# Optimization experiments

Measured on AMD Instinct MI355X. Metric: run time of the kernel, lower is better.

The kernel has to match this reference:

```python
import jax, jax.numpy as jnp
import numpy as np


def setup_inputs() -> dict:
    key = jax.random.key(0)
    k1, k2, k3 = jax.random.split(key, 3)
    B, c_in, T, N = 16, 64, 64, 512
    K, c_out = 3, 64
    x = jax.random.normal(k1, (B, c_in, T, N), dtype=jnp.float32)
    # scaled Laplacian-like matrix; scale to keep Chebyshev recurrence stable
    La = jax.random.normal(k2, (B, N, N), dtype=jnp.float32) / jnp.sqrt(jnp.float32(N))
    # Conv2d(K*c_in, c_out, 1x1, bias=False) weight, squeezed to [c_out, K*c_in]
    W = jax.random.normal(k3, (c_out, K * c_in), dtype=jnp.float32) * 0.05
    return {"x": x, "La": La, "W": W}


def reference(x, La, W):
    # x: [B, c_in, T, N], La: [B, N, N], W: [c_out, K*c_in]
    B, c_in, T, N = x.shape
    K = W.shape[1] // c_in
    xp = jnp.transpose(x, (0, 1, 3, 2))  # [B, c_in, N, T] -> 'bcnl'
    # Chebyshev polynomial recurrence: T0 = I, T1 = La, Tk = 2*La@T_{k-1} - T_{k-2}
    I = jnp.broadcast_to(jnp.eye(N, dtype=x.dtype), (B, N, N))
    Ls = [I, La]
    L0, L1 = I, La
    for _ in range(2, K):
        L2 = 2.0 * jnp.matmul(La, L1) - L0
        L0, L1 = L1, L2
        Ls.append(L2)
    Lap = jnp.stack(Ls, axis=1)            # [B, K, N, N]
    Lap = jnp.swapaxes(Lap, -1, -2)        # transpose(-1,-2) as in torch
    # graph conv: contract over source node n
    y = jnp.einsum('bcnl,bknq->bckql', xp, Lap)  # [B, c_in, K, N, T]
    y = y.reshape(B, c_in * K, N, T)       # channel index = c*K + k
    # 1x1 conv, no bias: [c_out, c_in*K] x [B, c_in*K, N, T]
    out = jnp.einsum('oi,binl->bonl', W, y)  # [B, c_out, N, T]
    out = jnp.transpose(out, (0, 1, 3, 2))   # [B, c_out, T, N]
    return out
```

## Files before the change

kernel.cpp:

```cpp
#include <hip/hip_runtime.h>
#include <hip/hip_bf16.h>


#define B_   16
#define CIN  64
#define T_   64
#define N_   512
#define M_   4096
#define KDIM 512
#define COUT 64

typedef __bf16 bf16x8 __attribute__((ext_vector_type(8)));
typedef float  floatx4 __attribute__((ext_vector_type(4)));

__device__ __forceinline__ float bf2f(unsigned short u) {
    unsigned int v = ((unsigned int)u) << 16;
    return __builtin_bit_cast(float, v);
}
__device__ __forceinline__ unsigned short f2bf(float f) {
    unsigned int u = __builtin_bit_cast(unsigned int, f);
    unsigned int lsb = (u >> 16) & 1u;
    u += 0x7fffu + lsb;
    return (unsigned short)(u >> 16);
}

#define GLOAD_LDS16(gp, lp)                                                  \
    __builtin_amdgcn_global_load_lds(                                        \
        (const __attribute__((address_space(1))) void*)(gp),                 \
        (__attribute__((address_space(3))) void*)(lp), 16, 0, 0)

__global__ __launch_bounds__(256) void cvt_f32_bf16(
    const float* __restrict__ src, unsigned short* __restrict__ dst, int n)
{
    int i = (blockIdx.x * 256 + threadIdx.x) * 8;
    if (i + 8 <= n) {
        float4 a = *(const float4*)(src + i);
        float4 b = *(const float4*)(src + i + 4);
        union { unsigned short s[8]; uint4 u; } o;
        o.s[0] = f2bf(a.x); o.s[1] = f2bf(a.y); o.s[2] = f2bf(a.z); o.s[3] = f2bf(a.w);
        o.s[4] = f2bf(b.x); o.s[5] = f2bf(b.y); o.s[6] = f2bf(b.z); o.s[7] = f2bf(b.w);
        *(uint4*)(dst + i) = o.u;
    }
}

__global__ __launch_bounds__(256) void cvt_la_dual(
    const float* __restrict__ La,
    unsigned short* __restrict__ Lab,
    unsigned short* __restrict__ LaT)
{
    __shared__ unsigned short t64[64][68];
    int b  = blockIdx.z;
    int r0 = blockIdx.y * 64;
    int c0 = blockIdx.x * 64;
    int t   = threadIdx.x;
    int row = t >> 2;
    int cg  = (t & 3) * 16;

    const float* src = La + (size_t)b * N_ * N_ + (size_t)(r0 + row) * N_ + c0 + cg;
    unsigned short s[16];
#pragma unroll
    for (int u = 0; u < 4; u++) {
        float4 f = *(const float4*)(src + u * 4);
        s[u * 4 + 0] = f2bf(f.x); s[u * 4 + 1] = f2bf(f.y);
        s[u * 4 + 2] = f2bf(f.z); s[u * 4 + 3] = f2bf(f.w);
    }
    union { unsigned short h[8]; uint4 u; } p0, p1;
#pragma unroll
    for (int u = 0; u < 8; u++) { p0.h[u] = s[u]; p1.h[u] = s[8 + u]; }
    unsigned short* d0 = Lab + (size_t)b * N_ * N_ + (size_t)(r0 + row) * N_ + c0 + cg;
    *(uint4*)d0 = p0.u;
    *(uint4*)(d0 + 8) = p1.u;
#pragma unroll
    for (int u = 0; u < 16; u++) t64[row][cg + u] = s[u];
    __syncthreads();
    int col = t >> 2;
    int rg  = (t & 3) * 16;
    union { unsigned short h[8]; uint4 u; } q0, q1;
#pragma unroll
    for (int u = 0; u < 8; u++) { q0.h[u] = t64[rg + u][col]; q1.h[u] = t64[rg + 8 + u][col]; }
    unsigned short* d1 = LaT + (size_t)b * N_ * N_ + (size_t)(c0 + col) * N_ + r0 + rg;
    *(uint4*)d1 = q0.u;
    *(uint4*)(d1 + 8) = q1.u;
}

__global__ __launch_bounds__(256) void pack_w(
    const float* __restrict__ W, unsigned short* __restrict__ Wb)
{
    int idx = threadIdx.x + blockIdx.x * 256;
    if (idx < 64 * 192) {
        int o = idx / 192, j = idx % 192;
        int c = j & 63, k = j >> 6;
        Wb[idx] = f2bf(W[o * 192 + c * 3 + k]);
    }
}

#define BM 128
#define BN 128
#define BK 32
#define KIT  (KDIM / BK)
#define SBUF (BM * BK)

__global__ __launch_bounds__(256) void gemm_la2(
    const unsigned short* __restrict__ A,
    const unsigned short* __restrict__ Bm,
    unsigned short* __restrict__ C)
{
    int h     = blockIdx.x;
    int g     = h & 7;
    int idx   = h >> 3;
    int batch = g * 2 + (idx >> 4);
    int local = idx & 15;
    int n0    = (local & 3) * BN;
    int m0    = (local >> 2) * BM;

    A  += (size_t)batch * N_ * KDIM;
    Bm += (size_t)batch * N_ * KDIM;
    C  += (size_t)batch * N_ * N_;

    __shared__ __align__(16) unsigned short As[3 * SBUF];
    __shared__ __align__(16) unsigned short Bs[3 * SBUF];

    int tid  = threadIdx.x;
    int lane = tid & 63;
    int wave = tid >> 6;
    int wm   = (wave >> 1) * 64;
    int wn   = (wave & 1) * 64;
    int l15  = lane & 15;
    int quad = lane >> 4;

    int r16 = lane >> 2;
    int sch = lane & 3;
    int gch = sch ^ ((r16 >> 1) & 3);

    const unsigned short* gA0 = A  + (size_t)(m0 + wave * 16 + r16) * KDIM + gch * 8;
    const unsigned short* gA1 = gA0 + (size_t)64 * KDIM;
    const unsigned short* gB0 = Bm + (size_t)(n0 + wave * 16 + r16) * KDIM + gch * 8;
    const unsigned short* gB1 = gB0 + (size_t)64 * KDIM;

    int dA0 = (wave * 16) * BK;
    int dA1 = (64 + wave * 16) * BK;

#define STAGE2(kk, bo) do {                                       \
        GLOAD_LDS16(gA0 + (kk) * BK, &As[(bo) + dA0]);            \
        GLOAD_LDS16(gA1 + (kk) * BK, &As[(bo) + dA1]);            \
        GLOAD_LDS16(gB0 + (kk) * BK, &Bs[(bo) + dA0]);            \
        GLOAD_LDS16(gB1 + (kk) * BK, &Bs[(bo) + dA1]);            \
    } while (0)

    int aoff[4], boff[4];
    int sl = quad ^ ((l15 >> 1) & 3);
#pragma unroll
    for (int im = 0; im < 4; im++) aoff[im] = (wm + im * 16 + l15) * BK + sl * 8;
#pragma unroll
    for (int jn = 0; jn < 4; jn++) boff[jn] = (wn + jn * 16 + l15) * BK + sl * 8;

    floatx4 acc[4][4];
#pragma unroll
    for (int i = 0; i < 4; i++)
#pragma unroll
        for (int j = 0; j < 4; j++) acc[i][j] = (floatx4)0.0f;

    STAGE2(0, 0);
    STAGE2(1, SBUF);

#pragma unroll
    for (int k = 0; k < KIT; ++k) {
        if (k < KIT - 1) asm volatile("s_waitcnt vmcnt(4)" ::: "memory");
        else             asm volatile("s_waitcnt vmcnt(0)" ::: "memory");
        __builtin_amdgcn_s_barrier();
        if (k + 2 < KIT) STAGE2(k + 2, ((k + 2) % 3) * SBUF);

        const int cb = (k % 3) * SBUF;
        bf16x8 af[4], bf[4];
#pragma unroll
        for (int im = 0; im < 4; im++)
            af[im] = __builtin_bit_cast(bf16x8, *(const uint4*)&As[cb + aoff[im]]);
#pragma unroll
        for (int jn = 0; jn < 4; jn++)
            bf[jn] = __builtin_bit_cast(bf16x8, *(const uint4*)&Bs[cb + boff[jn]]);
#pragma unroll
        for (int im = 0; im < 4; im++)
#pragma unroll
            for (int jn = 0; jn < 4; jn++)
                acc[im][jn] = __builtin_amdgcn_mfma_f32_16x16x32_bf16(
                    af[im], bf[jn], acc[im][jn], 0, 0, 0);
    }
#undef STAGE2

#pragma unroll
    for (int im = 0; im < 4; im++)
#pragma unroll
        for (int jn = 0; jn < 4; jn++) {
            int c = n0 + wn + jn * 16 + l15;
#pragma unroll
            for (int r = 0; r < 4; r++) {
                int m = m0 + wm + im * 16 + quad * 4 + r;
                C[(size_t)m * N_ + c] = f2bf(acc[im][jn][r]);
            }
        }
}

__global__ __launch_bounds__(256) void gemm_fused(
    const unsigned short* __restrict__ A,
    const unsigned short* __restrict__ B1,
    const unsigned short* __restrict__ B2,
    unsigned short* __restrict__ Z1,
    unsigned short* __restrict__ Z2)
{
    int h     = blockIdx.x;
    int g     = h & 7;
    int idx   = h >> 3;
    int batch = g * 2 + (idx >> 7);
    int local = idx & 127;
    int n0    = (local & 3) * BN;
    int m0    = (local >> 2) * BM;

    A  += (size_t)batch * M_ * KDIM;
    B1 += (size_t)batch * N_ * KDIM;
    B2 += (size_t)batch * N_ * KDIM;
    Z1 += (size_t)batch * M_ * N_;
    Z2 += (size_t)batch * M_ * N_;

    __shared__ __align__(16) unsigned short As [3 * SBUF];
    __shared__ __align__(16) unsigned short Bs1[3 * SBUF];
    __shared__ __align__(16) unsigned short Bs2[3 * SBUF];

    int tid  = threadIdx.x;
    int lane = tid & 63;
    int wave = tid >> 6;
    int wm   = (wave >> 1) * 64;
    int wn   = (wave & 1) * 64;
    int l15  = lane & 15;
    int quad = lane >> 4;

    int r16 = lane >> 2;
    int sch = lane & 3;
    int gch = sch ^ ((r16 >> 1) & 3);

    const unsigned short* gA0  = A  + (size_t)(m0 + wave * 16 + r16) * KDIM + gch * 8;
    const unsigned short* gA1  = gA0 + (size_t)64 * KDIM;
    const unsigned short* gB10 = B1 + (size_t)(n0 + wave * 16 + r16) * KDIM + gch * 8;
    const unsigned short* gB11 = gB10 + (size_t)64 * KDIM;
    const unsigned short* gB20 = B2 + (size_t)(n0 + wave * 16 + r16) * KDIM + gch * 8;
    const unsigned short* gB21 = gB20 + (size_t)64 * KDIM;

    int d0 = (wave * 16) * BK;
    int d1 = (64 + wave * 16) * BK;

#define STAGE6(kk, bo) do {                                        \
        GLOAD_LDS16(gA0  + (kk) * BK, &As [(bo) + d0]);            \
        GLOAD_LDS16(gA1  + (kk) * BK, &As [(bo) + d1]);            \
        GLOAD_LDS16(gB10 + (kk) * BK, &Bs1[(bo) + d0]);            \
        GLOAD_LDS16(gB11 + (kk) * BK, &Bs1[(bo) + d1]);            \
        GLOAD_LDS16(gB20 + (kk) * BK, &Bs2[(bo) + d0]);            \
        GLOAD_LDS16(gB21 + (kk) * BK, &Bs2[(bo) + d1]);            \
    } while (0)

    int aoff[4], boff[4];
    int sl = quad ^ ((l15 >> 1) & 3);
#pragma unroll
    for (int im = 0; im < 4; im++) aoff[im] = (wm + im * 16 + l15) * BK + sl * 8;
#pragma unroll
    for (int jn = 0; jn < 4; jn++) boff[jn] = (wn + jn * 16 + l15) * BK + sl * 8;

    floatx4 acc1[4][4], acc2[4][4];
#pragma unroll
    for (int i = 0; i < 4; i++)
#pragma unroll
        for (int j = 0; j < 4; j++) { acc1[i][j] = (floatx4)0.0f; acc2[i][j] = (floatx4)0.0f; }

    STAGE6(0, 0);
    STAGE6(1, SBUF);

#pragma unroll
    for (int k = 0; k < KIT; ++k) {
        if (k < KIT - 1) asm volatile("s_waitcnt vmcnt(6)" ::: "memory");
        else             asm volatile("s_waitcnt vmcnt(0)" ::: "memory");
        __builtin_amdgcn_s_barrier();
        if (k + 2 < KIT) STAGE6(k + 2, ((k + 2) % 3) * SBUF);

        const int cb = (k % 3) * SBUF;
        bf16x8 af[4], bf1[4], bf2[4];
#pragma unroll
        for (int im = 0; im < 4; im++)
            af[im] = __builtin_bit_cast(bf16x8, *(const uint4*)&As[cb + aoff[im]]);
#pragma unroll
        for (int jn = 0; jn < 4; jn++) {
            bf1[jn] = __builtin_bit_cast(bf16x8, *(const uint4*)&Bs1[cb + boff[jn]]);
            bf2[jn] = __builtin_bit_cast(bf16x8, *(const uint4*)&Bs2[cb + boff[jn]]);
        }
#pragma unroll
        for (int im = 0; im < 4; im++)
#pragma unroll
            for (int jn = 0; jn < 4; jn++) {
                acc1[im][jn] = __builtin_amdgcn_mfma_f32_16x16x32_bf16(
                    af[im], bf1[jn], acc1[im][jn], 0, 0, 0);
                acc2[im][jn] = __builtin_amdgcn_mfma_f32_16x16x32_bf16(
                    af[im], bf2[jn], acc2[im][jn], 0, 0, 0);
            }
    }
#undef STAGE6

    const unsigned short* Xb = A;
#pragma unroll
    for (int im = 0; im < 4; im++)
#pragma unroll
        for (int jn = 0; jn < 4; jn++) {
            int c = n0 + wn + jn * 16 + l15;
#pragma unroll
            for (int r = 0; r < 4; r++) {
                int m = m0 + wm + im * 16 + quad * 4 + r;
                size_t idx2 = (size_t)m * N_ + c;
                Z1[idx2] = f2bf(acc1[im][jn][r]);
                Z2[idx2] = f2bf(2.0f * acc2[im][jn][r] - bf2f(Xb[idx2]));
            }
        }
}

#define PJ_PITCH 40

__global__ __launch_bounds__(256) void proj(
    const unsigned short* __restrict__ xb,
    const unsigned short* __restrict__ z1b,
    const unsigned short* __restrict__ z2b,
    const unsigned short* __restrict__ Wb,
    float* __restrict__ out)
{
    __shared__ __align__(16) unsigned short Ds[256 * PJ_PITCH];

    int b  = blockIdx.y;
    int n0 = blockIdx.x * 256;
    int tid  = threadIdx.x;
    int lane = tid & 63;
    int wave = tid >> 6;
    int l15  = lane & 15;
    int quad = lane >> 4;

    size_t boff = (size_t)b * M_ * N_ + n0;
    const unsigned short* zp[3] = { xb + boff, z1b + boff, z2b + boff };

    bf16x8 wf[6];
#pragma unroll
    for (int kc = 0; kc < 6; kc++)
        wf[kc] = __builtin_bit_cast(bf16x8,
            *(const uint4*)(Wb + (size_t)(wave * 16 + l15) * 192 + kc * 32 + quad * 8));

    floatx4 acc[16];
#pragma unroll
    for (int i = 0; i < 16; i++) acc[i] = (floatx4)0.0f;

    int jl  = tid & 31;
    int nc0 = (tid >> 5) * 8;

    for (int kc = 0; kc < 6; kc++) {
        const unsigned short* src =
            zp[kc >> 1] + (size_t)((kc & 1) * 32 + jl) * (T_ * N_) + nc0;
        uint4 v[4];
#pragma unroll
        for (int u = 0; u < 4; u++) v[u] = *(const uint4*)(src + u * 64);

        __syncthreads();
#pragma unroll
        for (int u = 0; u < 4; u++) {
            unsigned short* d = &Ds[(size_t)(nc0 + u * 64) * PJ_PITCH + jl];
            unsigned int w0 = v[u].x, w1 = v[u].y, w2 = v[u].z, w3 = v[u].w;
            d[0 * PJ_PITCH] = (unsigned short)w0;
            d[1 * PJ_PITCH] = (unsigned short)(w0 >> 16);
            d[2 * PJ_PITCH] = (unsigned short)w1;
            d[3 * PJ_PITCH] = (unsigned short)(w1 >> 16);
            d[4 * PJ_PITCH] = (unsigned short)w2;
            d[5 * PJ_PITCH] = (unsigned short)(w2 >> 16);
            d[6 * PJ_PITCH] = (unsigned short)w3;
            d[7 * PJ_PITCH] = (unsigned short)(w3 >> 16);
        }
        __syncthreads();

#pragma unroll
        for (int nt = 0; nt < 16; nt++) {
            bf16x8 bfr = __builtin_bit_cast(bf16x8,
                *(const uint4*)(&Ds[(size_t)(nt * 16 + l15) * PJ_PITCH + quad * 8]));
            acc[nt] = __builtin_amdgcn_mfma_f32_16x16x32_bf16(wf[kc], bfr, acc[nt], 0, 0, 0);
        }
    }

    float* ob = out + (size_t)b * COUT * (T_ * N_);
#pragma unroll
    for (int nt = 0; nt < 16; nt++) {
        int n = n0 + nt * 16 + l15;
#pragma unroll
        for (int r = 0; r < 4; r++) {
            int o = wave * 16 + quad * 4 + r;
            ob[(size_t)o * (T_ * N_) + n] = acc[nt][r];
        }
    }
}

extern "C" void kernel_launch(void* const* d_in, const int* in_sizes, int n_in,
                              void* d_out, int out_size, void* d_ws, size_t ws_size,
                              hipStream_t stream) {
    const float* x  = (const float*)d_in[0];
    const float* La = (const float*)d_in[1];
    const float* W  = (const float*)d_in[2];
    float* out = (float*)d_out;

    const size_t n_x  = (size_t)B_ * CIN * T_ * N_;
    const size_t n_La = (size_t)B_ * N_ * N_;

    char* ws = (char*)d_ws;
    unsigned short* xb   = (unsigned short*)ws;
    unsigned short* Lab  = (unsigned short*)(ws + n_x * 2);
    unsigned short* z1b  = (unsigned short*)(ws + n_x * 2 + n_La * 2);
    unsigned short* z2b  = (unsigned short*)(ws + n_x * 4 + n_La * 2);
    unsigned short* Wb   = (unsigned short*)(ws + n_x * 6 + n_La * 2);
    unsigned short* LaT  = (unsigned short*)(ws + n_x * 6 + n_La * 2 + (1 << 20));
    unsigned short* La2b = (unsigned short*)(ws + n_x * 6 + n_La * 4 + (1 << 20));

    cvt_f32_bf16<<<(int)(n_x / 2048), 256, 0, stream>>>(x, xb, (int)n_x);
    cvt_la_dual<<<dim3(8, 8, 16), 256, 0, stream>>>(La, Lab, LaT);
    pack_w<<<48, 256, 0, stream>>>(W, Wb);

    gemm_la2<<<256, 256, 0, stream>>>(Lab, LaT, La2b);

    gemm_fused<<<2048, 256, 0, stream>>>(xb, Lab, La2b, z1b, z2b);

    dim3 gp((T_ * N_) / 256, B_);
    proj<<<gp, 256, 0, stream>>>(xb, z1b, z2b, Wb, out);
}
```

Measured before the change: 438.1 us.

## Apply channel-mix before graph GEMMs and fold identity term into output epilogue

The 1x1 channel projection is moved ahead of the graph convolution by linearity. The Chebyshev terms are folded into three premixed weight sets (W0-W2, W1, 2*W2), and x is mixed directly from fp32 into three bf16 tensors. A single GEMM then multiplies by La and La^2, adds the identity-term tensor, and writes fp32 output directly. This removes the separate x conversion, the z1/z2 intermediates and the proj kernel. The trade-off is the extra A operand stream in the GEMM, which drops to double buffering, and a different rounding order.

```diff
diff --git a/kernel.cpp b/kernel.cpp
--- a/kernel.cpp
+++ b/kernel.cpp
@@ -9,6 +9,7 @@
 #define M_   4096
 #define KDIM 512
 #define COUT 64
+#define LQ   32768
 
 typedef __bf16 bf16x8 __attribute__((ext_vector_type(8)));
 typedef float  floatx4 __attribute__((ext_vector_type(4)));
@@ -29,17 +30,18 @@
         (const __attribute__((address_space(1))) void*)(gp),                 \
         (__attribute__((address_space(3))) void*)(lp), 16, 0, 0)
 
-__global__ __launch_bounds__(256) void cvt_f32_bf16(
-    const float* __restrict__ src, unsigned short* __restrict__ dst, int n)
+__global__ __launch_bounds__(256) void pack_w3(
+    const float* __restrict__ W, unsigned short* __restrict__ Wp)
 {
-    int i = (blockIdx.x * 256 + threadIdx.x) * 8;
-    if (i + 8 <= n) {
-        float4 a = *(const float4*)(src + i);
-        float4 b = *(const float4*)(src + i + 4);
-        union { unsigned short s[8]; uint4 u; } o;
-        o.s[0] = f2bf(a.x); o.s[1] = f2bf(a.y); o.s[2] = f2bf(a.z); o.s[3] = f2bf(a.w);
-        o.s[4] = f2bf(b.x); o.s[5] = f2bf(b.y); o.s[6] = f2bf(b.z); o.s[7] = f2bf(b.w);
-        *(uint4*)(dst + i) = o.u;
+    int idx = blockIdx.x * 256 + threadIdx.x;
+    if (idx < 192 * 64) {
+        int op = idx >> 6, c = idx & 63;
+        int i = op >> 6, o = op & 63;
+        float v;
+        if (i == 0)      v = W[o * 192 + c * 3 + 0] - W[o * 192 + c * 3 + 2];
+        else if (i == 1) v = W[o * 192 + c * 3 + 1];
+        else             v = 2.0f * W[o * 192 + c * 3 + 2];
+        Wp[idx] = f2bf(v);
     }
 }
 
@@ -83,17 +85,6 @@
     *(uint4*)(d1 + 8) = q1.u;
 }
 
-__global__ __launch_bounds__(256) void pack_w(
-    const float* __restrict__ W, unsigned short* __restrict__ Wb)
-{
-    int idx = threadIdx.x + blockIdx.x * 256;
-    if (idx < 64 * 192) {
-        int o = idx / 192, j = idx % 192;
-        int c = j & 63, k = j >> 6;
-        Wb[idx] = f2bf(W[o * 192 + c * 3 + k]);
-    }
-}
-
 #define BM 128
 #define BN 128
 #define BK 32
@@ -200,12 +191,88 @@
         }
 }
 
-__global__ __launch_bounds__(256) void gemm_fused(
-    const unsigned short* __restrict__ A,
+__global__ __launch_bounds__(256) void chanmix(
+    const float* __restrict__ x,
+    const unsigned short* __restrict__ Wp,
+    unsigned short* __restrict__ y0,
+    unsigned short* __restrict__ y1,
+    unsigned short* __restrict__ y2)
+{
+    __shared__ __align__(16) unsigned short Xs[128 * 72];
+
+    int b  = blockIdx.y;
+    int l0 = blockIdx.x * 128;
+    int tid  = threadIdx.x;
+    int lane = tid & 63;
+    int wave = tid >> 6;
+    int l15  = lane & 15;
+    int quad = lane >> 4;
+
+    bf16x8 wf[3][2];
+#pragma unroll
+    for (int t3 = 0; t3 < 3; t3++)
+#pragma unroll
+        for (int ks = 0; ks < 2; ks++)
+            wf[t3][ks] = __builtin_bit_cast(bf16x8, *(const uint4*)(
+                Wp + (size_t)(wave * 48 + t3 * 16 + l15) * 64 + ks * 32 + quad * 8));
+
+    int cth  = tid & 63;
+    int lgrp = tid >> 6;
+    const float* xrow = x + ((size_t)b * CIN + cth) * LQ + l0 + lgrp * 32;
+#pragma unroll
+    for (int u = 0; u < 8; u++) {
+        float4 f = *(const float4*)(xrow + u * 4);
+        float fv[4] = { f.x, f.y, f.z, f.w };
+#pragma unroll
+        for (int j = 0; j < 4; j++) {
+            int ll = lgrp * 32 + u * 4 + j;
+            int p  = ((cth >> 3) + 2 * ll) & 7;
+            Xs[ll * 72 + p * 8 + (cth & 7)] = f2bf(fv[j]);
+        }
+    }
+    __syncthreads();
+
+    floatx4 acc[3][8];
+#pragma unroll
+    for (int i = 0; i < 3; i++)
+#pragma unroll
+        for (int j = 0; j < 8; j++) acc[i][j] = (floatx4)0.0f;
+
+#pragma unroll
+    for (int lf = 0; lf < 8; lf++) {
+        int lrow = lf * 16 + l15;
+#pragma unroll
+        for (int ks = 0; ks < 2; ks++) {
+            int p = ((ks * 4 + quad) + 2 * lrow) & 7;
+            bf16x8 bfr = __builtin_bit_cast(bf16x8,
+                *(const uint4*)&Xs[lrow * 72 + p * 8]);
+            acc[0][lf] = __builtin_amdgcn_mfma_f32_16x16x32_bf16(wf[0][ks], bfr, acc[0][lf], 0, 0, 0);
+            acc[1][lf] = __builtin_amdgcn_mfma_f32_16x16x32_bf16(wf[1][ks], bfr, acc[1][lf], 0, 0, 0);
+            acc[2][lf] = __builtin_amdgcn_mfma_f32_16x16x32_bf16(wf[2][ks], bfr, acc[2][lf], 0, 0, 0);
+        }
+    }
+
+#pragma unroll
+    for (int t3 = 0; t3 < 3; t3++) {
+        int opb = wave * 48 + t3 * 16;
+        unsigned short* yp = (opb < 64) ? y0 : ((opb < 128) ? y1 : y2);
+        int o = opb & 63;
+        unsigned short* dst = yp + ((size_t)b * 64 + o + quad * 4) * LQ + l0 + l15;
+#pragma unroll
+        for (int lf = 0; lf < 8; lf++)
+#pragma unroll
+            for (int r = 0; r < 4; r++)
+                dst[(size_t)r * LQ + lf * 16] = f2bf(acc[t3][lf][r]);
+    }
+}
+
+__global__ __launch_bounds__(256) void gemm_out(
+    const unsigned short* __restrict__ A1,
+    const unsigned short* __restrict__ A2,
     const unsigned short* __restrict__ B1,
     const unsigned short* __restrict__ B2,
-    unsigned short* __restrict__ Z1,
-    unsigned short* __restrict__ Z2)
+    const unsigned short* __restrict__ Y0,
+    float* __restrict__ out)
 {
     int h     = blockIdx.x;
     int g     = h & 7;
@@ -215,15 +282,17 @@
     int n0    = (local & 3) * BN;
     int m0    = (local >> 2) * BM;
 
-    A  += (size_t)batch * M_ * KDIM;
+    A1 += (size_t)batch * M_ * KDIM;
+    A2 += (size_t)batch * M_ * KDIM;
     B1 += (size_t)batch * N_ * KDIM;
     B2 += (size_t)batch * N_ * KDIM;
-    Z1 += (size_t)batch * M_ * N_;
-    Z2 += (size_t)batch * M_ * N_;
-
-    __shared__ __align__(16) unsigned short As [3 * SBUF];
-    __shared__ __align__(16) unsigned short Bs1[3 * SBUF];
-    __shared__ __align__(16) unsigned short Bs2[3 * SBUF];
+    Y0 += (size_t)batch * M_ * N_;
+    out += (size_t)batch * M_ * N_;
+
+    __shared__ __align__(16) unsigned short As1[2 * SBUF];
+    __shared__ __align__(16) unsigned short As2[2 * SBUF];
+    __shared__ __align__(16) unsigned short Bs1[2 * SBUF];
+    __shared__ __align__(16) unsigned short Bs2[2 * SBUF];
 
     int tid  = threadIdx.x;
     int lane = tid & 63;
@@ -237,8 +306,10 @@
     int sch = lane & 3;
     int gch = sch ^ ((r16 >> 1) & 3);
 
-    const unsigned short* gA0  = A  + (size_t)(m0 + wave * 16 + r16) * KDIM + gch * 8;
-    const unsigned short* gA1  = gA0 + (size_t)64 * KDIM;
+    const unsigned short* gA10 = A1 + (size_t)(m0 + wave * 16 + r16) * KDIM + gch * 8;
+    const unsigned short* gA11 = gA10 + (size_t)64 * KDIM;
+    const unsigned short* gA20 = A2 + (size_t)(m0 + wave * 16 + r16) * KDIM + gch * 8;
+    const unsigned short* gA21 = gA20 + (size_t)64 * KDIM;
     const unsigned short* gB10 = B1 + (size_t)(n0 + wave * 16 + r16) * KDIM + gch * 8;
     const unsigned short* gB11 = gB10 + (size_t)64 * KDIM;
     const unsigned short* gB20 = B2 + (size_t)(n0 + wave * 16 + r16) * KDIM + gch * 8;
@@ -247,9 +318,11 @@
     int d0 = (wave * 16) * BK;
     int d1 = (64 + wave * 16) * BK;
 
-#define STAGE6(kk, bo) do {                                        \
-        GLOAD_LDS16(gA0  + (kk) * BK, &As [(bo) + d0]);            \
-        GLOAD_LDS16(gA1  + (kk) * BK, &As [(bo) + d1]);            \
+#define STAGE8(kk, bo) do {                                        \
+        GLOAD_LDS16(gA10 + (kk) * BK, &As1[(bo) + d0]);            \
+        GLOAD_LDS16(gA11 + (kk) * BK, &As1[(bo) + d1]);            \
+        GLOAD_LDS16(gA20 + (kk) * BK, &As2[(bo) + d0]);            \
+        GLOAD_LDS16(gA21 + (kk) * BK, &As2[(bo) + d1]);            \
         GLOAD_LDS16(gB10 + (kk) * BK, &Bs1[(bo) + d0]);            \
         GLOAD_LDS16(gB11 + (kk) * BK, &Bs1[(bo) + d1]);            \
         GLOAD_LDS16(gB20 + (kk) * BK, &Bs2[(bo) + d0]);            \
@@ -269,39 +342,40 @@
 #pragma unroll
         for (int j = 0; j < 4; j++) { acc1[i][j] = (floatx4)0.0f; acc2[i][j] = (floatx4)0.0f; }
 
-    STAGE6(0, 0);
-    STAGE6(1, SBUF);
+    STAGE8(0, 0);
 
 #pragma unroll
     for (int k = 0; k < KIT; ++k) {
-        if (k < KIT - 1) asm volatile("s_waitcnt vmcnt(6)" ::: "memory");
+        __builtin_amdgcn_s_barrier();
+        if (k + 1 < KIT) STAGE8(k + 1, ((k + 1) & 1) * SBUF);
+        if (k + 1 < KIT) asm volatile("s_waitcnt vmcnt(8)" ::: "memory");
         else             asm volatile("s_waitcnt vmcnt(0)" ::: "memory");
         __builtin_amdgcn_s_barrier();
-        if (k + 2 < KIT) STAGE6(k + 2, ((k + 2) % 3) * SBUF);
-
-        const int cb = (k % 3) * SBUF;
-        bf16x8 af[4], bf1[4], bf2[4];
-#pragma unroll
-        for (int im = 0; im < 4; im++)
-            af[im] = __builtin_bit_cast(bf16x8, *(const uint4*)&As[cb + aoff[im]]);
+
+        const int cb = (k & 1) * SBUF;
+        bf16x8 a1[4], a2[4], b1[4], b2[4];
+#pragma unroll
+        for (int im = 0; im < 4; im++) {
+            a1[im] = __builtin_bit_cast(bf16x8, *(const uint4*)&As1[cb + aoff[im]]);
+            a2[im] = __builtin_bit_cast(bf16x8, *(const uint4*)&As2[cb + aoff[im]]);
+        }
 #pragma unroll
         for (int jn = 0; jn < 4; jn++) {
-            bf1[jn] = __builtin_bit_cast(bf16x8, *(const uint4*)&Bs1[cb + boff[jn]]);
-            bf2[jn] = __builtin_bit_cast(bf16x8, *(const uint4*)&Bs2[cb + boff[jn]]);
+            b1[jn] = __builtin_bit_cast(bf16x8, *(const uint4*)&Bs1[cb + boff[jn]]);
+            b2[jn] = __builtin_bit_cast(bf16x8, *(const uint4*)&Bs2[cb + boff[jn]]);
         }
 #pragma unroll
         for (int im = 0; im < 4; im++)
 #pragma unroll
             for (int jn = 0; jn < 4; jn++) {
                 acc1[im][jn] = __builtin_amdgcn_mfma_f32_16x16x32_bf16(
-                    af[im], bf1[jn], acc1[im][jn], 0, 0, 0);
+                    a1[im], b1[jn], acc1[im][jn], 0, 0, 0);
                 acc2[im][jn] = __builtin_amdgcn_mfma_f32_16x16x32_bf16(
-                    af[im], bf2[jn], acc2[im][jn], 0, 0, 0);
+                    a2[im], b2[jn], acc2[im][jn], 0, 0, 0);
             }
     }
-#undef STAGE6
-
-    const unsigned short* Xb = A;
+#undef STAGE8
+
 #pragma unroll
     for (int im = 0; im < 4; im++)
 #pragma unroll
@@ -311,88 +385,9 @@
             for (int r = 0; r < 4; r++) {
                 int m = m0 + wm + im * 16 + quad * 4 + r;
                 size_t idx2 = (size_t)m * N_ + c;
-                Z1[idx2] = f2bf(acc1[im][jn][r]);
-                Z2[idx2] = f2bf(2.0f * acc2[im][jn][r] - bf2f(Xb[idx2]));
+                out[idx2] = acc1[im][jn][r] + acc2[im][jn][r] + bf2f(Y0[idx2]);
             }
         }
-}
-
-#define PJ_PITCH 40
-
-__global__ __launch_bounds__(256) void proj(
-    const unsigned short* __restrict__ xb,
-    const unsigned short* __restrict__ z1b,
-    const unsigned short* __restrict__ z2b,
-    const unsigned short* __restrict__ Wb,
-    float* __restrict__ out)
-{
-    __shared__ __align__(16) unsigned short Ds[256 * PJ_PITCH];
-
-    int b  = blockIdx.y;
-    int n0 = blockIdx.x * 256;
-    int tid  = threadIdx.x;
-    int lane = tid & 63;
-    int wave = tid >> 6;
-    int l15  = lane & 15;
-    int quad = lane >> 4;
-
-    size_t boff = (size_t)b * M_ * N_ + n0;
-    const unsigned short* zp[3] = { xb + boff, z1b + boff, z2b + boff };
-
-    bf16x8 wf[6];
-#pragma unroll
-    for (int kc = 0; kc < 6; kc++)
-        wf[kc] = __builtin_bit_cast(bf16x8,
-            *(const uint4*)(Wb + (size_t)(wave * 16 + l15) * 192 + kc * 32 + quad * 8));
-
-    floatx4 acc[16];
-#pragma unroll
-    for (int i = 0; i < 16; i++) acc[i] = (floatx4)0.0f;
-
-    int jl  = tid & 31;
-    int nc0 = (tid >> 5) * 8;
-
-    for (int kc = 0; kc < 6; kc++) {
-        const unsigned short* src =
-            zp[kc >> 1] + (size_t)((kc & 1) * 32 + jl) * (T_ * N_) + nc0;
-        uint4 v[4];
-#pragma unroll
-        for (int u = 0; u < 4; u++) v[u] = *(const uint4*)(src + u * 64);
-
-        __syncthreads();
-#pragma unroll
-        for (int u = 0; u < 4; u++) {
-            unsigned short* d = &Ds[(size_t)(nc0 + u * 64) * PJ_PITCH + jl];
-            unsigned int w0 = v[u].x, w1 = v[u].y, w2 = v[u].z, w3 = v[u].w;
-            d[0 * PJ_PITCH] = (unsigned short)w0;
-            d[1 * PJ_PITCH] = (unsigned short)(w0 >> 16);
-            d[2 * PJ_PITCH] = (unsigned short)w1;
-            d[3 * PJ_PITCH] = (unsigned short)(w1 >> 16);
-            d[4 * PJ_PITCH] = (unsigned short)w2;
-            d[5 * PJ_PITCH] = (unsigned short)(w2 >> 16);
-            d[6 * PJ_PITCH] = (unsigned short)w3;
-            d[7 * PJ_PITCH] = (unsigned short)(w3 >> 16);
-        }
-        __syncthreads();
-
-#pragma unroll
-        for (int nt = 0; nt < 16; nt++) {
-            bf16x8 bfr = __builtin_bit_cast(bf16x8,
-                *(const uint4*)(&Ds[(size_t)(nt * 16 + l15) * PJ_PITCH + quad * 8]));
-            acc[nt] = __builtin_amdgcn_mfma_f32_16x16x32_bf16(wf[kc], bfr, acc[nt], 0, 0, 0);
-        }
-    }
-
-    float* ob = out + (size_t)b * COUT * (T_ * N_);
-#pragma unroll
-    for (int nt = 0; nt < 16; nt++) {
-        int n = n0 + nt * 16 + l15;
-#pragma unroll
-        for (int r = 0; r < 4; r++) {
-            int o = wave * 16 + quad * 4 + r;
-            ob[(size_t)o * (T_ * N_) + n] = acc[nt][r];
-        }
-    }
 }
 
 extern "C" void kernel_launch(void* const* d_in, const int* in_sizes, int n_in,
@@ -407,22 +402,19 @@
     const size_t n_La = (size_t)B_ * N_ * N_;
 
     char* ws = (char*)d_ws;
-    unsigned short* xb   = (unsigned short*)ws;
-    unsigned short* Lab  = (unsigned short*)(ws + n_x * 2);
-    unsigned short* z1b  = (unsigned short*)(ws + n_x * 2 + n_La * 2);
-    unsigned short* z2b  = (unsigned short*)(ws + n_x * 4 + n_La * 2);
-    unsigned short* Wb   = (unsigned short*)(ws + n_x * 6 + n_La * 2);
-    unsigned short* LaT  = (unsigned short*)(ws + n_x * 6 + n_La * 2 + (1 << 20));
-    unsigned short* La2b = (unsigned short*)(ws + n_x * 6 + n_La * 4 + (1 << 20));
-
-    cvt_f32_bf16<<<(int)(n_x / 2048), 256, 0, stream>>>(x, xb, (int)n_x);
+    unsigned short* y0b  = (unsigned short*)ws;
+    unsigned short* y1b  = (unsigned short*)(ws + n_x * 2);
+    unsigned short* y2b  = (unsigned short*)(ws + n_x * 4);
+    unsigned short* Lab  = (unsigned short*)(ws + n_x * 6);
+    unsigned short* LaT  = (unsigned short*)(ws + n_x * 6 + n_La * 2);
+    unsigned short* La2b = (unsigned short*)(ws + n_x * 6 + n_La * 4);
+    unsigned short* Wp   = (unsigned short*)(ws + n_x * 6 + n_La * 6);
+
+    pack_w3<<<48, 256, 0, stream>>>(W, Wp);
     cvt_la_dual<<<dim3(8, 8, 16), 256, 0, stream>>>(La, Lab, LaT);
-    pack_w<<<48, 256, 0, stream>>>(W, Wb);
-
     gemm_la2<<<256, 256, 0, stream>>>(Lab, LaT, La2b);
 
-    gemm_fused<<<2048, 256, 0, stream>>>(xb, Lab, La2b, z1b, z2b);
-
-    dim3 gp((T_ * N_) / 256, B_);
-    proj<<<gp, 256, 0, stream>>>(xb, z1b, z2b, Wb, out);
-}
+    chanmix<<<dim3(LQ / 128, B_), 256, 0, stream>>>(x, Wp, y0b, y1b, y2b);
+
+    gemm_out<<<2048, 256, 0, stream>>>(y1b, y2b, Lab, La2b, y0b, out);
+}
```

After: 524.0 us. 19.6% more time.
